# Performance work log

Hardware: AMD Instinct MI355X
Metric: run time of the kernel (lower is better)

## Reference

```python
import jax, jax.numpy as jnp
import numpy as np

H = 2880
E = 8
K = 2
FF = 2880
CLIP = 7.0
AUX_COEF = 0.01
INIT_STD = 0.02
B, T = 2, 1024


def setup_inputs() -> dict:
    key = jax.random.key(0)
    ks = jax.random.split(key, 4)
    x = jax.random.normal(ks[0], (B, T, H), dtype=jnp.float32)
    W_in = INIT_STD * jax.random.normal(ks[1], (E, H, 2 * FF), dtype=jnp.float32)
    b_in = jnp.zeros((E, 2 * FF), dtype=jnp.float32)
    W_out = INIT_STD * jax.random.normal(ks[2], (E, FF, H), dtype=jnp.float32)
    b_out = jnp.zeros((E, H), dtype=jnp.float32)
    router_w = INIT_STD * jax.random.normal(ks[3], (E, H), dtype=jnp.float32)
    router_b = jnp.zeros((E,), dtype=jnp.float32)
    return {"x": x, "W_in": W_in, "b_in": b_in, "W_out": W_out,
            "b_out": b_out, "router_w": router_w, "router_b": router_b}


def reference(x, W_in, b_in, W_out, b_out, router_w, router_b):
    Bx, Tx, Hx = x.shape
    x_flat = x.reshape(-1, Hx)                       # [S, H]
    logits = x_flat @ router_w.T + router_b          # [S, E]

    topk_w, topk_idx = jax.lax.top_k(logits, K)      # [S, K]
    topk_w = jax.nn.softmax(topk_w.astype(jnp.float32), axis=-1).astype(x.dtype)
    one_hot = jax.nn.one_hot(topk_idx, E, dtype=x.dtype)        # [S, K, E]
    final_w = (one_hot * topk_w[..., None]).sum(axis=1)          # [S, E]

    probs = jax.nn.softmax(logits.astype(jnp.float32), axis=-1)  # [S, E]
    importance = probs.mean(axis=0)
    load = final_w.astype(jnp.float32).mean(axis=0)
    aux_loss = AUX_COEF * E * (importance * load).sum()

    # Dense over all experts (as in the original module)
    expert_in = jnp.einsum('sh,ehd->sed', x_flat, W_in) + b_in   # [S, E, 2FF]
    up, gate = jnp.split(expert_in, 2, axis=-1)
    up = jnp.clip(up, -CLIP, CLIP)
    gate = jnp.clip(gate, -CLIP, CLIP)
    act = jax.nn.silu(gate) * up                                 # [S, E, FF]
    expert_out = jnp.einsum('sef,efh->seh', act, W_out) + b_out  # [S, E, H]
    out = jnp.einsum('seh,se->sh', expert_out, final_w).reshape(Bx, Tx, Hx)

    expert_utilization = final_w.mean(axis=0)
    router_entropy = -(probs * jnp.log(probs + 1e-10)).sum(axis=-1).mean()
    return out, aux_loss, expert_utilization, router_entropy
```

## Files before the change

### kernel.cpp

```cpp
#include <hip/hip_runtime.h>
#include <hip/hip_bf16.h>
#include <cstdint>
#include <cstddef>

#define H_ 2880
#define E_ 8
#define FF_ 2880
#define TWO_FF 5760
#define S_ 2048
#define NPAD 5120
#define CLIPV 7.0f
#define AUXC 0.01f
#define NKB 45

#define GRID1 1280
#define CPX1  160
#define GRID2 640
#define CPX2  80

typedef __attribute__((ext_vector_type(8))) short bf16x8;
typedef __attribute__((ext_vector_type(4))) float f32x4;

#define WS_COUNTS   0
#define WS_FILL     32
#define WS_BASEP    64
#define WS_NS       104
#define WS_SCHED_E  128
#define WS_SCHED_C  5248
#define WS_SCHED_R  10368
#define WS_SCH2_E   15488
#define WS_SCH2_C   18048
#define WS_SCH2_R   20608
#define WS_IDX2     23168
#define WS_W2       39552
#define WS_PROBS    55936
#define WS_ENT      121472
#define WS_TOKL     129664
#define WS_ASSW     150144
#define WS_AG       262144
#define WS_TIN      29753344
#define WS_ACT      295174144
#define WS_TOUT     262144

typedef const __attribute__((address_space(1))) void global_cvoid;
typedef __attribute__((address_space(3))) void lds_void;

__device__ __forceinline__ void gload_lds16(const void* g, void* l) {
  __builtin_amdgcn_global_load_lds((global_cvoid*)g, (lds_void*)l, 16, 0, 0);
}

__device__ __forceinline__ unsigned int pack2bf(float a, float b) {
  __hip_bfloat162 h = __float22bfloat162_rn(make_float2(a, b));
  union { __hip_bfloat162 h; unsigned int u; } c; c.h = h; return c.u;
}

__device__ __forceinline__ unsigned short f2bf1(float f) {
  __hip_bfloat16 h = __float2bfloat16(f);
  union { __hip_bfloat16 h; unsigned short u; } c; c.h = h; return c.u;
}

__global__ void k_router(const float* __restrict__ x, const float* __restrict__ rw,
                         const float* __restrict__ rb, int* __restrict__ counts,
                         int* __restrict__ idx2, float* __restrict__ wtop,
                         float* __restrict__ probs, float* __restrict__ ent) {
  int wave = threadIdx.x >> 6, lane = threadIdx.x & 63;
  int s = blockIdx.x * 4 + wave;
  if (s >= S_) return;
  const float* xr = x + (size_t)s * H_;
  float acc[E_];
#pragma unroll
  for (int e = 0; e < E_; ++e) acc[e] = 0.f;
  for (int k = lane; k < H_; k += 64) {
    float xv = xr[k];
#pragma unroll
    for (int e = 0; e < E_; ++e) acc[e] = fmaf(xv, rw[e * H_ + k], acc[e]);
  }
#pragma unroll
  for (int e = 0; e < E_; ++e) {
#pragma unroll
    for (int off = 32; off > 0; off >>= 1) acc[e] += __shfl_xor(acc[e], off, 64);
    acc[e] += rb[e];
  }
  if (lane == 0) {
    int i1 = 0; float v1 = acc[0];
#pragma unroll
    for (int e = 1; e < E_; ++e) if (acc[e] > v1) { v1 = acc[e]; i1 = e; }
    int i2 = -1; float v2 = -3.4e38f;
#pragma unroll
    for (int e = 0; e < E_; ++e) if (e != i1 && acc[e] > v2) { v2 = acc[e]; i2 = e; }
    float w1 = 1.f / (1.f + expf(v2 - v1));
    float w2v = 1.f - w1;
    float m = v1;
    float se = 0.f; float p[E_];
#pragma unroll
    for (int e = 0; e < E_; ++e) { p[e] = expf(acc[e] - m); se += p[e]; }
    float inv = 1.f / se; float ents = 0.f;
#pragma unroll
    for (int e = 0; e < E_; ++e) {
      p[e] *= inv;
      ents -= p[e] * logf(p[e] + 1e-10f);
      probs[(size_t)s * E_ + e] = p[e];
    }
    ent[s] = ents;
    idx2[2 * s] = i1; idx2[2 * s + 1] = i2;
    wtop[2 * s] = w1; wtop[2 * s + 1] = w2v;
    atomicAdd(&counts[i1], 1); atomicAdd(&counts[i2], 1);
  }
}

__global__ void k_finalize(const int* __restrict__ counts, const float* __restrict__ probs,
                           const float* __restrict__ ent, const int* __restrict__ idx2,
                           const float* __restrict__ wtop, float* __restrict__ outsc,
                           int* __restrict__ basep, int* __restrict__ sched_e,
                           int* __restrict__ sched_c, int* __restrict__ sched_r,
                           int* __restrict__ s2e, int* __restrict__ s2c,
                           int* __restrict__ s2r, int* __restrict__ nsp) {
  __shared__ float red[256];
  __shared__ float tot[17];
  int t = threadIdx.x;
  float imp[8], ld[8]; float es = 0.f;
#pragma unroll
  for (int e = 0; e < 8; ++e) { imp[e] = 0.f; ld[e] = 0.f; }
  for (int s = t; s < S_; s += 256) {
#pragma unroll
    for (int e = 0; e < 8; ++e) imp[e] += probs[(size_t)s * 8 + e];
    es += ent[s];
    int e0 = idx2[2 * s], e1 = idx2[2 * s + 1];
    float a = wtop[2 * s], b = wtop[2 * s + 1];
#pragma unroll
    for (int e = 0; e < 8; ++e)
      ld[e] += (e0 == e ? a : 0.f) + (e1 == e ? b : 0.f);
  }
#pragma unroll
  for (int q = 0; q < 17; ++q) {
    float v = (q < 8) ? imp[q] : ((q < 16) ? ld[q - 8] : es);
    red[t] = v; __syncthreads();
    for (int o = 128; o > 0; o >>= 1) { if (t < o) red[t] += red[t + o]; __syncthreads(); }
    if (t == 0) tot[q] = red[0];
    __syncthreads();
  }
  if (t == 0) {
    float aux = 0.f;
#pragma unroll
    for (int e = 0; e < 8; ++e) aux += (tot[e] / (float)S_) * (tot[8 + e] / (float)S_);
    aux *= AUXC * (float)E_;
    outsc[0] = aux;
#pragma unroll
    for (int e = 0; e < 8; ++e) outsc[1 + e] = tot[8 + e] / (float)S_;
    outsc[9] = tot[16] / (float)S_;
    int bp = 0;
    for (int e = 0; e < 8; ++e) {
      basep[e] = bp;
      bp += ((counts[e] + 127) >> 7) << 7;
    }
    basep[8] = bp;
    int ns = 0;
    for (int e = 0; e < 8; ++e) {
      int tc = (counts[e] + 127) >> 7;
      for (int col = 0; col < 30; ++col)
        for (int tt = 0; tt < tc; ++tt) {
          sched_e[ns] = e; sched_c[ns] = col; sched_r[ns] = tt * 128; ++ns;
        }
    }
    nsp[0] = ns;
    int n2 = 0;
    for (int e = 0; e < 8; ++e) {
      int tc = (counts[e] + 127) >> 7;
      for (int col = 0; col < 15; ++col)
        for (int tt = 0; tt < tc; ++tt) {
          s2e[n2] = e; s2c[n2] = col; s2r[n2] = tt * 128; ++n2;
        }
    }
    nsp[1] = n2;
  }
}

__global__ void k_fill(const int* __restrict__ idx2, const float* __restrict__ wtop,
                       const int* __restrict__ basep, int* __restrict__ fill,
                       int* __restrict__ tokl, float* __restrict__ assw) {
  int s = blockIdx.x * 256 + threadIdx.x;
  if (s >= S_) return;
#pragma unroll
  for (int k = 0; k < 2; ++k) {
    int e = idx2[2 * s + k];
    int p = basep[e] + atomicAdd(&fill[e], 1);
    tokl[p] = s;
    assw[p] = wtop[2 * s + k];
  }
}

__global__ void k_gather(const float* __restrict__ x, const int* __restrict__ tokl,
                         unsigned short* __restrict__ Ag) {
  int g = blockIdx.x;
  int tok = tokl[g];
  int tm = g >> 7, r = g & 127;
  unsigned short* dst = Ag + (size_t)tm * 45 * 8192;
  const float* src = x + (size_t)tok * H_;
  for (int c = threadIdx.x; c < 360; c += 256) {
    float4 v0 = *(const float4*)(src + c * 8);
    float4 v1 = *(const float4*)(src + c * 8 + 4);
    uint4 o;
    o.x = pack2bf(v0.x, v0.y); o.y = pack2bf(v0.z, v0.w);
    o.z = pack2bf(v1.x, v1.y); o.w = pack2bf(v1.z, v1.w);
    *(uint4*)(dst + (size_t)(c >> 3) * 8192 + (c & 7) * 1024 + r * 8) = o;
  }
}

template <int LD>
__device__ __forceinline__ void convw_body(const float* __restrict__ src,
                                           unsigned short* __restrict__ dst,
                                           float (*ls)[97]) {
  int tid = threadIdx.x;
#pragma unroll
  for (int i = 0; i < 6; ++i) {
    int u = tid + 256 * i;
    int r = u / 24, c4 = u % 24;
    float4 v = *(const float4*)(src + (size_t)r * LD + c4 * 4);
    ls[r][c4 * 4 + 0] = v.x; ls[r][c4 * 4 + 1] = v.y;
    ls[r][c4 * 4 + 2] = v.z; ls[r][c4 * 4 + 3] = v.w;
  }
  __syncthreads();
#pragma unroll
  for (int i = 0; i < 3; ++i) {
    int ci = tid + 256 * i;
    int kq = ci / 96, n = ci % 96;
    float f[8];
#pragma unroll
    for (int j = 0; j < 8; ++j) f[j] = ls[kq * 8 + j][n];
    uint4 o;
    o.x = pack2bf(f[0], f[1]); o.y = pack2bf(f[2], f[3]);
    o.z = pack2bf(f[4], f[5]); o.w = pack2bf(f[6], f[7]);
    *(uint4*)(dst + ci * 8) = o;
  }
}

__global__ __launch_bounds__(256) void k_convw_in(const float* __restrict__ Win,
                                                  unsigned short* __restrict__ Tin) {
  __shared__ float ls[64][97];
  int bid = blockIdx.x;
  int e = bid / 2700, r = bid % 2700, nt = r / 45, kb = r % 45;
  const float* src = Win + (size_t)e * H_ * TWO_FF + (size_t)kb * 64 * TWO_FF + nt * 96;
  unsigned short* dst = Tin + (((size_t)e * 60 + nt) * 45 + kb) * 6144;
  convw_body<TWO_FF>(src, dst, ls);
}

__global__ __launch_bounds__(256) void k_convw_out(const float* __restrict__ Wout,
                                                   unsigned short* __restrict__ Tout) {
  __shared__ float ls[64][97];
  int bid = blockIdx.x;
  int e = bid / 1350, r = bid % 1350, nt = r / 45, kb = r % 45;
  const float* src = Wout + (size_t)e * FF_ * H_ + (size_t)kb * 64 * H_ + nt * 96;
  unsigned short* dst = Tout + (((size_t)e * 30 + nt) * 45 + kb) * 6144;
  convw_body<H_>(src, dst, ls);
}

__global__ __launch_bounds__(256, 2) void k_gemm1(
    const unsigned short* __restrict__ Ag, const unsigned short* __restrict__ Tin,
    const float* __restrict__ bin, const int* __restrict__ sched_e,
    const int* __restrict__ sched_c, const int* __restrict__ sched_r,
    const int* __restrict__ basep, const int* __restrict__ counts,
    const int* __restrict__ nsp, unsigned short* __restrict__ act) {
  __shared__ __align__(16) char lds[81920];
  int lid = (blockIdx.x & 7) * CPX1 + (blockIdx.x >> 3);
  if (lid >= nsp[0]) return;
  int e = sched_e[lid], col = sched_c[lid], row0 = sched_r[lid];
  int n_e = counts[e], rbase = basep[e];
  int n0 = col * 96;
  int tid = threadIdx.x, lane = tid & 63, wv = tid >> 6;
  int wm = wv >> 1, wn = wv & 1;
  int tile_m = (rbase + row0) >> 7;

  const char* abase  = (const char*)Ag  + (size_t)tile_m * 45 * 16384;
  const char* bubase = (const char*)Tin + (((size_t)e * 60 + col) * 45) * 12288;
  const char* bgbase = (const char*)Tin + (((size_t)e * 60 + col + 30) * 45) * 12288;

#define ST1(BUF, KT) do {                                                        \
  const char* at_ = abase + (size_t)(KT) * 16384;                                \
  const char* bu_ = bubase + (size_t)(KT) * 12288;                               \
  const char* bg_ = bgbase + (size_t)(KT) * 12288;                               \
  _Pragma("unroll") for (int i_ = 0; i_ < 4; ++i_)                               \
    gload_lds16(at_ + (wv * 4 + i_) * 1024 + lane * 16,                          \
                lds + (BUF) * 16384 + (wv * 4 + i_) * 1024);                     \
  _Pragma("unroll") for (int i_ = 0; i_ < 3; ++i_) {                             \
    gload_lds16(bu_ + (wv * 3 + i_) * 1024 + lane * 16,                          \
                lds + 32768 + (BUF) * 12288 + (wv * 3 + i_) * 1024);             \
    gload_lds16(bg_ + (wv * 3 + i_) * 1024 + lane * 16,                          \
                lds + 57344 + (BUF) * 12288 + (wv * 3 + i_) * 1024); }           \
} while (0)

  f32x4 aU[4][3], aG[4][3];
#pragma unroll
  for (int m = 0; m < 4; ++m)
#pragma unroll
    for (int n = 0; n < 3; ++n) { aU[m][n] = (f32x4)0.f; aG[m][n] = (f32x4)0.f; }

  ST1(0, 0);
  __syncthreads();
  int cur = 0;
  for (int kt = 0; kt < NKB; ++kt) {
    if (kt + 1 < NKB) ST1(cur ^ 1, kt + 1);
    const char* Ab  = lds + cur * 16384 + (lane >> 4) * 2048 + (wm * 64 + (lane & 15)) * 16;
    const char* Bub = lds + 32768 + cur * 12288 + (lane >> 4) * 1536 + (wn * 48 + (lane & 15)) * 16;
    const char* Bgb = Bub + 24576;
#pragma unroll
    for (int s = 0; s < 2; ++s) {
      bf16x8 af[4], bu[3], bg[3];
#pragma unroll
      for (int m = 0; m < 4; ++m) af[m] = *(const bf16x8*)(Ab + s * 8192 + m * 256);
#pragma unroll
      for (int n = 0; n < 3; ++n) {
        bu[n] = *(const bf16x8*)(Bub + s * 6144 + n * 256);
        bg[n] = *(const bf16x8*)(Bgb + s * 6144 + n * 256);
      }
#pragma unroll
      for (int n = 0; n < 3; ++n)
#pragma unroll
        for (int m = 0; m < 4; ++m) {
          aU[m][n] = __builtin_amdgcn_mfma_f32_16x16x32_bf16(af[m], bu[n], aU[m][n], 0, 0, 0);
          aG[m][n] = __builtin_amdgcn_mfma_f32_16x16x32_bf16(af[m], bg[n], aG[m][n], 0, 0, 0);
        }
    }
    __syncthreads();
    cur ^= 1;
  }
#undef ST1

  float bias_u[3], bias_g[3];
#pragma unroll
  for (int n = 0; n < 3; ++n) {
    int cidx = n0 + wn * 48 + n * 16 + (lane & 15);
    bias_u[n] = bin[(size_t)e * TWO_FF + cidx];
    bias_g[n] = bin[(size_t)e * TWO_FF + FF_ + cidx];
  }
  unsigned short* atile = act + (size_t)tile_m * 45 * 8192;
#pragma unroll
  for (int m = 0; m < 4; ++m) {
#pragma unroll
    for (int q = 0; q < 4; ++q) {
      int r = wm * 64 + m * 16 + (lane >> 4) * 4 + q;
      if (row0 + r < n_e) {
#pragma unroll
        for (int n = 0; n < 3; ++n) {
          int cidx = n0 + wn * 48 + n * 16 + (lane & 15);
          float u = aU[m][n][q] + bias_u[n];
          float g = aG[m][n][q] + bias_g[n];
          u = fminf(fmaxf(u, -CLIPV), CLIPV);
          g = fminf(fmaxf(g, -CLIPV), CLIPV);
          float sig = 1.f / (1.f + expf(-g));
          atile[(size_t)(cidx >> 6) * 8192 + ((cidx >> 3) & 7) * 1024 + r * 8 + (cidx & 7)]
              = f2bf1(g * sig * u);
        }
      }
    }
  }
}

__global__ __launch_bounds__(256, 2) void k_gemm2(
    const unsigned short* __restrict__ act, const unsigned short* __restrict__ Tout,
    const float* __restrict__ bout, const int* __restrict__ s2e,
    const int* __restrict__ s2c, const int* __restrict__ s2r,
    const int* __restrict__ basep, const int* __restrict__ counts,
    const int* __restrict__ nsp, const int* __restrict__ tokl,
    const float* __restrict__ assw, float* __restrict__ out) {
  __shared__ __align__(16) char lds[81920];
  int lid = (blockIdx.x & 7) * CPX2 + (blockIdx.x >> 3);
  if (lid >= nsp[1]) return;
  int e = s2e[lid], col = s2c[lid], row0 = s2r[lid];
  int n_e = counts[e], rbase = basep[e];
  int n0 = col * 192;
  int tid = threadIdx.x, lane = tid & 63, wv = tid >> 6;
  int wm = wv >> 1, wn = wv & 1;
  int tile_m = (rbase + row0) >> 7;

  const char* abase = (const char*)act + (size_t)tile_m * 45 * 16384;
  const char* bbase = (const char*)Tout + (((size_t)e * 30 + col * 2) * 45) * 12288;

#define ST2(BUF, KT) do {                                                        \
  const char* at_ = abase + (size_t)(KT) * 16384;                                \
  _Pragma("unroll") for (int i_ = 0; i_ < 4; ++i_)                               \
    gload_lds16(at_ + (wv * 4 + i_) * 1024 + lane * 16,                          \
                lds + (BUF) * 16384 + (wv * 4 + i_) * 1024);                     \
  _Pragma("unroll") for (int i_ = 0; i_ < 6; ++i_) {                             \
    int ch_ = wv * 6 + i_;                                                       \
    const char* bt_ = bbase + (size_t)(ch_ / 12) * 45 * 12288                    \
                      + (size_t)(KT) * 12288 + (ch_ % 12) * 1024;                \
    gload_lds16(bt_ + lane * 16, lds + 32768 + (BUF) * 24576 + ch_ * 1024); }    \
} while (0)

  f32x4 acc[4][6];
#pragma unroll
  for (int m = 0; m < 4; ++m)
#pragma unroll
    for (int n = 0; n < 6; ++n) acc[m][n] = (f32x4)0.f;

  ST2(0, 0);
  __syncthreads();
  int cur = 0;
  for (int kt = 0; kt < NKB; ++kt) {
    if (kt + 1 < NKB) ST2(cur ^ 1, kt + 1);
    const char* Ab = lds + cur * 16384 + (lane >> 4) * 2048 + (wm * 64 + (lane & 15)) * 16;
    const char* Bb = lds + 32768 + cur * 24576 + wn * 12288 + (lane >> 4) * 1536 + (lane & 15) * 16;
#pragma unroll
    for (int s = 0; s < 2; ++s) {
      bf16x8 af[4], bf[6];
#pragma unroll
      for (int m = 0; m < 4; ++m) af[m] = *(const bf16x8*)(Ab + s * 8192 + m * 256);
#pragma unroll
      for (int n = 0; n < 6; ++n) bf[n] = *(const bf16x8*)(Bb + s * 6144 + n * 256);
#pragma unroll
      for (int n = 0; n < 6; ++n)
#pragma unroll
        for (int m = 0; m < 4; ++m)
          acc[m][n] = __builtin_amdgcn_mfma_f32_16x16x32_bf16(af[m], bf[n], acc[m][n], 0, 0, 0);
    }
    __syncthreads();
    cur ^= 1;
  }
#undef ST2

  float bb[6];
#pragma unroll
  for (int n = 0; n < 6; ++n)
    bb[n] = bout[(size_t)e * H_ + n0 + wn * 96 + n * 16 + (lane & 15)];
#pragma unroll
  for (int m = 0; m < 4; ++m) {
#pragma unroll
    for (int q = 0; q < 4; ++q) {
      int r = wm * 64 + m * 16 + (lane >> 4) * 4 + q;
      if (row0 + r < n_e) {
        int g = rbase + row0 + r;
        int tok = tokl[g];
        float w = assw[g];
        float* orow = out + (size_t)tok * H_;
#pragma unroll
        for (int n = 0; n < 6; ++n) {
          int cidx = n0 + wn * 96 + n * 16 + (lane & 15);
          atomicAdd(&orow[cidx], w * (acc[m][n][q] + bb[n]));
        }
      }
    }
  }
}

extern "C" void kernel_launch(void* const* d_in, const int* in_sizes, int n_in,
                              void* d_out, int out_size, void* d_ws, size_t ws_size,
                              hipStream_t stream) {
  (void)in_sizes; (void)n_in; (void)ws_size;
  const float* x        = (const float*)d_in[0];
  const float* W_in     = (const float*)d_in[1];
  const float* b_in     = (const float*)d_in[2];
  const float* W_out    = (const float*)d_in[3];
  const float* b_out    = (const float*)d_in[4];
  const float* router_w = (const float*)d_in[5];
  const float* router_b = (const float*)d_in[6];
  float* out = (float*)d_out;
  char* ws = (char*)d_ws;

  int*   counts  = (int*)(ws + WS_COUNTS);
  int*   fill    = (int*)(ws + WS_FILL);
  int*   basep   = (int*)(ws + WS_BASEP);
  int*   nsp     = (int*)(ws + WS_NS);
  int*   sched_e = (int*)(ws + WS_SCHED_E);
  int*   sched_c = (int*)(ws + WS_SCHED_C);
  int*   sched_r = (int*)(ws + WS_SCHED_R);
  int*   s2e     = (int*)(ws + WS_SCH2_E);
  int*   s2c     = (int*)(ws + WS_SCH2_C);
  int*   s2r     = (int*)(ws + WS_SCH2_R);
  int*   idx2    = (int*)(ws + WS_IDX2);
  float* wtop    = (float*)(ws + WS_W2);
  float* probs   = (float*)(ws + WS_PROBS);
  float* ent     = (float*)(ws + WS_ENT);
  int*   tokl    = (int*)(ws + WS_TOKL);
  float* assw    = (float*)(ws + WS_ASSW);
  unsigned short* Ag   = (unsigned short*)(ws + WS_AG);
  unsigned short* Tin  = (unsigned short*)(ws + WS_TIN);
  unsigned short* actp = (unsigned short*)(ws + WS_ACT);
  unsigned short* Tout = (unsigned short*)(ws + WS_TOUT);

  hipMemsetAsync(ws + WS_COUNTS, 0, 128, stream);
  hipMemsetAsync(ws + WS_TOKL, 0, NPAD * 4, stream);
  hipMemsetAsync(d_out, 0, (size_t)out_size * sizeof(float), stream);

  k_router<<<S_ / 4, 256, 0, stream>>>(x, router_w, router_b, counts, idx2, wtop, probs, ent);
  k_finalize<<<1, 256, 0, stream>>>(counts, probs, ent, idx2, wtop,
                                    out + (size_t)S_ * H_, basep, sched_e, sched_c, sched_r,
                                    s2e, s2c, s2r, nsp);
  k_fill<<<S_ / 256, 256, 0, stream>>>(idx2, wtop, basep, fill, tokl, assw);
  k_gather<<<NPAD, 256, 0, stream>>>(x, tokl, Ag);
  k_convw_in<<<21600, 256, 0, stream>>>(W_in, Tin);
  k_gemm1<<<GRID1, 256, 0, stream>>>(Ag, Tin, b_in, sched_e, sched_c, sched_r,
                                     basep, counts, nsp, actp);
  k_convw_out<<<10800, 256, 0, stream>>>(W_out, Tout);
  k_gemm2<<<GRID2, 256, 0, stream>>>(actp, Tout, b_out, s2e, s2c, s2r,
                                     basep, counts, nsp, tokl, assw, out);
}
```

Measured before the change: 755.3 us.

## Use partial vmcnt waits to overlap prefetch, balance XCD block mapping

```diff
diff --git a/kernel.cpp b/kernel.cpp
--- a/kernel.cpp
+++ b/kernel.cpp
@@ -14,9 +14,7 @@
 #define NKB 45
 
 #define GRID1 1280
-#define CPX1  160
 #define GRID2 640
-#define CPX2  80
 
 typedef __attribute__((ext_vector_type(8))) short bf16x8;
 typedef __attribute__((ext_vector_type(4))) float f32x4;
@@ -59,6 +57,14 @@
   union { __hip_bfloat16 h; unsigned short u; } c; c.h = h; return c.u;
 }
 
+__device__ __forceinline__ int xcd_lid(int bid, int ns) {
+  int q = ns >> 3, r = ns & 7;
+  int xcd = bid & 7, i = bid >> 3;
+  int cnt = q + (xcd < r ? 1 : 0);
+  if (i >= cnt) return -1;
+  return xcd * q + (xcd < r ? xcd : r) + i;
+}
+
 __global__ void k_router(const float* __restrict__ x, const float* __restrict__ rw,
                          const float* __restrict__ rb, int* __restrict__ counts,
                          int* __restrict__ idx2, float* __restrict__ wtop,
@@ -261,8 +267,8 @@
     const int* __restrict__ basep, const int* __restrict__ counts,
     const int* __restrict__ nsp, unsigned short* __restrict__ act) {
   __shared__ __align__(16) char lds[81920];
-  int lid = (blockIdx.x & 7) * CPX1 + (blockIdx.x >> 3);
-  if (lid >= nsp[0]) return;
+  int lid = xcd_lid(blockIdx.x, nsp[0]);
+  if (lid < 0) return;
   int e = sched_e[lid], col = sched_c[lid], row0 = sched_r[lid];
   int n_e = counts[e], rbase = basep[e];
   int n0 = col * 96;
@@ -295,10 +301,16 @@
     for (int n = 0; n < 3; ++n) { aU[m][n] = (f32x4)0.f; aG[m][n] = (f32x4)0.f; }
 
   ST1(0, 0);
-  __syncthreads();
   int cur = 0;
   for (int kt = 0; kt < NKB; ++kt) {
-    if (kt + 1 < NKB) ST1(cur ^ 1, kt + 1);
+    asm volatile("s_barrier" ::: "memory");
+    if (kt + 1 < NKB) {
+      ST1(cur ^ 1, kt + 1);
+      asm volatile("s_waitcnt vmcnt(10)" ::: "memory");
+    } else {
+      asm volatile("s_waitcnt vmcnt(0)" ::: "memory");
+    }
+    asm volatile("s_barrier" ::: "memory");
     const char* Ab  = lds + cur * 16384 + (lane >> 4) * 2048 + (wm * 64 + (lane & 15)) * 16;
     const char* Bub = lds + 32768 + cur * 12288 + (lane >> 4) * 1536 + (wn * 48 + (lane & 15)) * 16;
     const char* Bgb = Bub + 24576;
@@ -320,7 +332,6 @@
           aG[m][n] = __builtin_amdgcn_mfma_f32_16x16x32_bf16(af[m], bg[n], aG[m][n], 0, 0, 0);
         }
     }
-    __syncthreads();
     cur ^= 1;
   }
 #undef ST1
@@ -363,8 +374,8 @@
     const int* __restrict__ nsp, const int* __restrict__ tokl,
     const float* __restrict__ assw, float* __restrict__ out) {
   __shared__ __align__(16) char lds[81920];
-  int lid = (blockIdx.x & 7) * CPX2 + (blockIdx.x >> 3);
-  if (lid >= nsp[1]) return;
+  int lid = xcd_lid(blockIdx.x, nsp[1]);
+  if (lid < 0) return;
   int e = s2e[lid], col = s2c[lid], row0 = s2r[lid];
   int n_e = counts[e], rbase = basep[e];
   int n0 = col * 192;
@@ -394,10 +405,16 @@
     for (int n = 0; n < 6; ++n) acc[m][n] = (f32x4)0.f;
 
   ST2(0, 0);
-  __syncthreads();
   int cur = 0;
   for (int kt = 0; kt < NKB; ++kt) {
-    if (kt + 1 < NKB) ST2(cur ^ 1, kt + 1);
+    asm volatile("s_barrier" ::: "memory");
+    if (kt + 1 < NKB) {
+      ST2(cur ^ 1, kt + 1);
+      asm volatile("s_waitcnt vmcnt(10)" ::: "memory");
+    } else {
+      asm volatile("s_waitcnt vmcnt(0)" ::: "memory");
+    }
+    asm volatile("s_barrier" ::: "memory");
     const char* Ab = lds + cur * 16384 + (lane >> 4) * 2048 + (wm * 64 + (lane & 15)) * 16;
     const char* Bb = lds + 32768 + cur * 24576 + wn * 12288 + (lane >> 4) * 1536 + (lane & 15) * 16;
 #pragma unroll
@@ -413,7 +430,6 @@
         for (int m = 0; m < 4; ++m)
           acc[m][n] = __builtin_amdgcn_mfma_f32_16x16x32_bf16(af[m], bf[n], acc[m][n], 0, 0, 0);
     }
-    __syncthreads();
     cur ^= 1;
   }
 #undef ST2
```

After: 707.2 us. -6.4%, faster.
